# Kernel tuning notes

Measured on AMD Instinct MI355X. Metric: run time of the kernel, lower is better.

## Reference

```python
import jax, jax.numpy as jnp
import numpy as np

MAX_WAVELENGTH = 1000.0

def _sine_pos(n, d):
    # keras_nlp SinePositionEncoding with max_wavelength=1000
    pos = jnp.arange(n, dtype=jnp.float32)
    i = jnp.arange(d)
    timescales = (1.0 / MAX_WAVELENGTH) ** ((2 * (i // 2)).astype(jnp.float32) / d)
    ang = pos[:, None] * timescales[None, :]  # (n, d)
    return jnp.where(i % 2 == 0, jnp.sin(ang), jnp.cos(ang))


def setup_inputs() -> dict:
    key = jax.random.key(0)
    ks = jax.random.split(key, 6)
    B, N, D, H, O = 4, 2048, 512, 8, 64
    inputs = jax.random.normal(ks[0], (B, N, D), jnp.float32)
    mem = jax.random.normal(ks[1], (B, H, O, O), jnp.float32) * 0.02
    # z accumulates sums of (elu(k)+1) > 0, so keep it positive
    z = jax.random.uniform(ks[2], (B, H, O), jnp.float32) + 1.0
    attn_kernel = jax.random.normal(ks[3], (D, H, O, 3), jnp.float32) * (1.0 / np.sqrt(D))
    out_kernel = jax.random.normal(ks[4], (O, H, O), jnp.float32) * (1.0 / np.sqrt(O * H))
    beta = jnp.zeros((1,), jnp.float32)
    return dict(inputs=inputs, mem=mem, z=z, attn_kernel=attn_kernel,
                out_kernel=out_kernel, beta=beta)


def reference(inputs, mem, z, attn_kernel, out_kernel, beta):
    B, N, D = inputs.shape
    x = inputs + _sine_pos(N, D)[None].astype(inputs.dtype)
    # fused QKV projection: (B,N,H,dims,3)
    kvq = jnp.einsum('bni,ihok->bnhok', x, attn_kernel)
    k, v, q = kvq[..., 0], kvq[..., 1], kvq[..., 2]
    # linear-attention memory readout
    q_elu = jax.nn.elu(q) + 1.0
    num = jnp.einsum('bhdo,bnhd->bnho', mem, q_elu)
    den = jnp.einsum('bhd,bnhd->bnh', z, q_elu)[..., None] + 1e-8
    A_mem = num / den
    # delta-rule state update
    k_elu = jax.nn.elu(k) + 1.0
    next_mem = mem + jnp.einsum('bnhz,bnho->bhzo', k_elu, v - A_mem)
    next_z = z + k_elu.sum(axis=1)
    # causal softmax attention over the chunk
    scale = jnp.sqrt(jnp.asarray(D, inputs.dtype))
    qk = jnp.einsum('bnho,bkho->bhnk', q, k) / scale
    mask = -(1.0 - jnp.tril(jnp.ones((N, N), inputs.dtype))) * 1e10
    A_soft = jax.nn.softmax(qk + mask, axis=-1)
    A_dot = jnp.einsum('bhnk,bkho->bnho', A_soft, v)
    # sigmoid-gated mix + output projection
    g = jax.nn.sigmoid(beta)  # (1,) broadcasts
    A = g * A_mem + (1.0 - g) * A_dot
    out = jnp.einsum('bnhi,iho->bno', A, out_kernel)
    return out, next_mem, next_z
```

## Files before the change

### kernel.cpp

```cpp
#include <hip/hip_runtime.h>
#include <hip/hip_bf16.h>
#include <math.h>

#define BB 4
#define SEQ 2048
#define DIM 512
#define NH 8
#define HD 64

typedef __attribute__((ext_vector_type(8))) short short8;
typedef __attribute__((ext_vector_type(4))) float f32x4;
typedef __attribute__((ext_vector_type(2))) unsigned int u32x2;
typedef __attribute__((address_space(3))) const ushort lds_cushort;

static __device__ inline ushort f2bf(float f) {
    __hip_bfloat16 h = __float2bfloat16(f);
    union { __hip_bfloat16 h; ushort u; } cv;
    cv.h = h;
    return cv.u;
}
static __device__ inline float bf2f(ushort u) {
    return __uint_as_float((uint)u << 16);
}

#define GLOAD16(g, l)                                                          \
    __builtin_amdgcn_global_load_lds(                                          \
        (const __attribute__((address_space(1))) uint32_t*)(g),                \
        (__attribute__((address_space(3))) uint32_t*)(l), 16, 0, 0)

static __device__ __forceinline__ u32x2 tr16_b64(lds_cushort* p) {
    u32x2 r;
    asm volatile("ds_read_b64_tr_b16 %0, %1" : "=v"(r) : "v"(p) : "memory");
    return r;
}

__global__ __launch_bounds__(256) void pos_add_bf16_kernel(const float* __restrict__ in,
                                                           ushort* __restrict__ xbf) {
    int idx = blockIdx.x * 256 + threadIdx.x;
    int p = idx & 255;
    int n = (idx >> 8) & 2047;
    float e = (float)(2 * p) * (1.0f / 512.0f);
    float ts = __expf(-6.907755278982137f * e);
    float arev = (float)n * (ts * 0.15915494309189535f);
    float f = arev - floorf(arev);
    float s = __builtin_amdgcn_sinf(f);
    float c = __builtin_amdgcn_cosf(f);
    float2 v = *(const float2*)(in + (size_t)idx * 2);
    uint pack = (uint)f2bf(v.x + s) | ((uint)f2bf(v.y + c) << 16);
    ((uint*)xbf)[idx] = pack;
}

__global__ __launch_bounds__(256) void wprep_kernel(const float* __restrict__ w,
                                                    ushort* __restrict__ wt,
                                                    const float* __restrict__ wo,
                                                    ushort* __restrict__ wobf) {
    int bid = blockIdx.x;
    int t = threadIdx.x;
    if (bid < 96) {
        __shared__ float tile[64][129];
        int ib = bid & 7;
        int jb = bid >> 3;
        #pragma unroll
        for (int u = 0; u < 8; ++u) {
            int idx = u * 1024 + t * 4;
            int r = idx >> 7, j = idx & 127;
            float4 v = *(const float4*)(w + (size_t)(ib * 64 + r) * 1536 + jb * 128 + j);
            tile[r][j] = v.x; tile[r][j + 1] = v.y; tile[r][j + 2] = v.z; tile[r][j + 3] = v.w;
        }
        __syncthreads();
        int j = t >> 1;
        int rh = (t & 1) * 32;
        int jg = jb * 128 + j;
        int h = jg / 192;
        int rem = jg - h * 192;
        int o = rem / 3;
        int c = rem - o * 3;
        int nrow = c * 512 + h * 64 + o;
        #pragma unroll
        for (int s8 = 0; s8 < 4; ++s8) {
            short8 pk;
            #pragma unroll
            for (int q = 0; q < 8; ++q) pk[q] = (short)f2bf(tile[rh + s8 * 8 + q][j]);
            *(short8*)(wt + (size_t)nrow * 512 + ib * 64 + rh + s8 * 8) = pk;
        }
    } else {
        int g = (bid - 96) * 256 + t;
        int o2 = g >> 9, k = g & 511;
        int h = k >> 6, i = k & 63;
        wobf[g] = f2bf(wo[(size_t)i * 512 + h * 64 + o2]);
    }
}

__global__ __launch_bounds__(256) void qkv_mfma_kernel(const ushort* __restrict__ xbf,
                                                       const ushort* __restrict__ wt,
                                                       ushort* __restrict__ kbf,
                                                       ushort* __restrict__ vbf,
                                                       ushort* __restrict__ qbf) {
    __shared__ __align__(16) ushort As[128 * 64];
    __shared__ __align__(16) ushort Bs[128 * 64];
    int t = threadIdx.x;
    int w = t >> 6, lane = t & 63, l15 = lane & 15, lg = lane >> 4;
    int wr = w >> 1, wc = w & 1;
    int m0 = blockIdx.x * 128;
    int by = blockIdx.y;
    int n0 = by * 128;
    int sw = l15 & 7;
    f32x4 acc[4][4] = {};

    int rowp[4], colp[4];
    #pragma unroll
    for (int p = 0; p < 4; ++p) {
        int ch = t + 256 * p;
        rowp[p] = ch >> 3;
        colp[p] = (((ch & 7) ^ (rowp[p] & 7))) * 8;
    }

    for (int k0 = 0; k0 < 512; k0 += 64) {
        __syncthreads();
        #pragma unroll
        for (int p = 0; p < 4; ++p)
            GLOAD16(xbf + (size_t)(m0 + rowp[p]) * 512 + k0 + colp[p], As + (t + 256 * p) * 8);
        #pragma unroll
        for (int p = 0; p < 4; ++p)
            GLOAD16(wt + (size_t)(n0 + rowp[p]) * 512 + k0 + colp[p], Bs + (t + 256 * p) * 8);
        __syncthreads();
        #pragma unroll
        for (int ks = 0; ks < 2; ++ks) {
            short8 af[4], bf[4];
            #pragma unroll
            for (int mi = 0; mi < 4; ++mi)
                af[mi] = *(const short8*)&As[(wr * 64 + mi * 16 + l15) * 64 + ((ks * 4 + lg) ^ sw) * 8];
            #pragma unroll
            for (int ni = 0; ni < 4; ++ni)
                bf[ni] = *(const short8*)&Bs[(wc * 64 + ni * 16 + l15) * 64 + ((ks * 4 + lg) ^ sw) * 8];
            #pragma unroll
            for (int mi = 0; mi < 4; ++mi)
                #pragma unroll
                for (int ni = 0; ni < 4; ++ni)
                    acc[mi][ni] = __builtin_amdgcn_mfma_f32_16x16x32_bf16(af[mi], bf[ni], acc[mi][ni], 0, 0, 0);
        }
    }

    ushort* dst = (by < 4) ? kbf : (by < 8) ? vbf : qbf;
    int ho0 = (by & 3) * 128 + wc * 64;
    int mb = m0 + wr * 64;
    #pragma unroll
    for (int mi = 0; mi < 4; ++mi)
        #pragma unroll
        for (int ni = 0; ni < 4; ++ni)
            #pragma unroll
            for (int r = 0; r < 4; ++r)
                dst[(size_t)(mb + mi * 16 + lg * 4 + r) * 512 + ho0 + ni * 16 + l15] =
                    f2bf(acc[mi][ni][r]);
}

__global__ __launch_bounds__(256) void amem_mfma_kernel(const ushort* __restrict__ qbf,
                                                        const float* __restrict__ mem,
                                                        const float* __restrict__ zin,
                                                        ushort* __restrict__ ambf) {
    int bid = blockIdx.x;
    int nt = bid & 7;
    int h = (bid >> 3) & 7;
    int b = bid >> 6;
    __shared__ __align__(16) ushort bt_s[80 * 64];
    int t = threadIdx.x;
    int w = t >> 6, lane = t & 63, l15 = lane & 15, lg = lane >> 4;

    {
        int d = t >> 2;
        int o0 = (t & 3) * 16;
        const float* msrc = mem + (size_t)(b * 8 + h) * 4096 + (size_t)d * 64 + o0;
        #pragma unroll
        for (int j = 0; j < 16; ++j) {
            int o = o0 + j;
            int c = (d >> 3) ^ (o & 7);
            bt_s[(o * 8 + c) * 8 + (d & 7)] = f2bf(msrc[j]);
        }
        if (t < 64) {
            bt_s[(64 * 8 + (t >> 3)) * 8 + (t & 7)] = f2bf(zin[(b * 8 + h) * 64 + t]);
        }
    }
    __syncthreads();

    int sw = l15 & 7;
    short8 bfr[5][2];
    #pragma unroll
    for (int n = 0; n < 5; ++n) {
        const ushort* br = &bt_s[(n * 16 + l15) * 64];
        bfr[n][0] = *(const short8*)&br[(lg ^ sw) * 8];
        bfr[n][1] = *(const short8*)&br[((4 + lg) ^ sw) * 8];
    }

    int rowbase = b * 2048 + nt * 256 + w * 64;
    f32x4 acc[4][5] = {};
    #pragma unroll
    for (int m = 0; m < 4; ++m) {
        const ushort* qrow = qbf + (size_t)(rowbase + m * 16 + l15) * 512 + h * 64;
        short8 q0 = *(const short8*)(qrow + lg * 8);
        short8 q1 = *(const short8*)(qrow + 32 + lg * 8);
        short8 a0, a1;
        #pragma unroll
        for (int j = 0; j < 8; ++j) {
            float f0 = bf2f((ushort)q0[j]);
            float f1 = bf2f((ushort)q1[j]);
            a0[j] = (short)f2bf(f0 > 0.f ? f0 + 1.f : __expf(f0));
            a1[j] = (short)f2bf(f1 > 0.f ? f1 + 1.f : __expf(f1));
        }
        #pragma unroll
        for (int n = 0; n < 5; ++n) {
            acc[m][n] = __builtin_amdgcn_mfma_f32_16x16x32_bf16(a0, bfr[n][0], acc[m][n], 0, 0, 0);
            acc[m][n] = __builtin_amdgcn_mfma_f32_16x16x32_bf16(a1, bfr[n][1], acc[m][n], 0, 0, 0);
        }
    }

    #pragma unroll
    for (int m = 0; m < 4; ++m) {
        float inv[4];
        #pragma unroll
        for (int r = 0; r < 4; ++r) {
            float d = __shfl(acc[m][4][r], (lane & 48));
            inv[r] = 1.f / (d + 1e-8f);
        }
        #pragma unroll
        for (int r = 0; r < 4; ++r) {
            ushort* dst = ambf + (size_t)(rowbase + m * 16 + lg * 4 + r) * 512 + h * 64;
            #pragma unroll
            for (int n = 0; n < 4; ++n)
                dst[n * 16 + l15] = f2bf(acc[m][n][r] * inv[r]);
        }
    }
}

__global__ __launch_bounds__(256) void delta_part_kernel(const ushort* __restrict__ kbf,
                                                         const ushort* __restrict__ vbf,
                                                         const ushort* __restrict__ ambf,
                                                         float* __restrict__ part,
                                                         float* __restrict__ zpart) {
    int bid = blockIdx.x;
    int bh = bid & 31;
    int chunk = bid >> 5;
    int h = bh & 7, b = bh >> 3;
    __shared__ __align__(16) float ke_s[2048];
    __shared__ __align__(16) float vm_s[2048];
    int t = threadIdx.x;
    int tx = t & 15, ty = t >> 4;
    float acc[4][4] = {};
    float nz = 0.f;
    int nbase = chunk * 256;
    for (int n0 = 0; n0 < 256; n0 += 32) {
        {
            int nn = t >> 3, cc = (t & 7) * 8;
            size_t g = (size_t)(b * 2048 + nbase + n0 + nn) * 512 + h * 64 + cc;
            short8 k8 = *(const short8*)(kbf + g);
            short8 v8 = *(const short8*)(vbf + g);
            short8 a8 = *(const short8*)(ambf + g);
            #pragma unroll
            for (int j = 0; j < 8; ++j) {
                float kv = bf2f((ushort)k8[j]);
                ke_s[t * 8 + j] = kv > 0.f ? kv + 1.f : __expf(kv);
                vm_s[t * 8 + j] = bf2f((ushort)v8[j]) - bf2f((ushort)a8[j]);
            }
        }
        __syncthreads();
        #pragma unroll
        for (int nn = 0; nn < 32; ++nn) {
            float4 ka4 = *(const float4*)&ke_s[nn * 64 + ty * 4];
            float4 vv4 = *(const float4*)&vm_s[nn * 64 + tx * 4];
            float ka[4] = {ka4.x, ka4.y, ka4.z, ka4.w};
            float vv[4] = {vv4.x, vv4.y, vv4.z, vv4.w};
            #pragma unroll
            for (int i = 0; i < 4; ++i)
                #pragma unroll
                for (int j = 0; j < 4; ++j) acc[i][j] += ka[i] * vv[j];
        }
        if (t < 64) {
            #pragma unroll
            for (int nn = 0; nn < 32; ++nn) nz += ke_s[nn * 64 + t];
        }
        __syncthreads();
    }
    float* pdst = part + (size_t)bid * 4096;
    #pragma unroll
    for (int i = 0; i < 4; ++i)
        #pragma unroll
        for (int j = 0; j < 4; ++j)
            pdst[(ty * 4 + i) * 64 + tx * 4 + j] = acc[i][j];
    if (t < 64) zpart[bid * 64 + t] = nz;
}

__global__ __launch_bounds__(256) void delta_reduce_kernel(const float* __restrict__ part,
                                                           const float* __restrict__ zpart,
                                                           const float* __restrict__ mem,
                                                           const float* __restrict__ zin,
                                                           float* __restrict__ out_mem,
                                                           float* __restrict__ out_z) {
    int bh = blockIdx.x;
    int t = threadIdx.x;
    #pragma unroll
    for (int q = 0; q < 4; ++q) {
        int e = t * 16 + q * 4;
        float4 acc = *(const float4*)(mem + (size_t)bh * 4096 + e);
        #pragma unroll
        for (int c = 0; c < 8; ++c) {
            float4 pv = *(const float4*)(part + (size_t)(c * 32 + bh) * 4096 + e);
            acc.x += pv.x; acc.y += pv.y; acc.z += pv.z; acc.w += pv.w;
        }
        *(float4*)(out_mem + (size_t)bh * 4096 + e) = acc;
    }
    if (t < 64) {
        float z = zin[bh * 64 + t];
        #pragma unroll
        for (int c = 0; c < 8; ++c) z += zpart[(c * 32 + bh) * 64 + t];
        out_z[bh * 64 + t] = z;
    }
}

__global__ __launch_bounds__(256, 2) void flash5_kernel(const ushort* __restrict__ qbf,
                                                        const ushort* __restrict__ kbf,
                                                        const ushort* __restrict__ vbf,
                                                        ushort* __restrict__ adbf) {
    int bid0 = blockIdx.x;
    int bid = (bid0 & 7) * 64 + (bid0 >> 3);
    int i = bid & 15;
    int h = (bid >> 4) & 7;
    int b = bid >> 7;
    __shared__ __align__(16) ushort k_s[2][4096];
    __shared__ __align__(16) ushort v_s[2][4096];
    __shared__ __align__(16) ushort p_s[4][1024];
    int t = threadIdx.x;
    int w = t >> 6, lane = t & 63, l15 = lane & 15, lg = lane >> 4;
    const int rA = i, rB = 31 - i;
    const int sw = l15 & 7;
    const float C = 0.06375875f;

    const ushort* qbase = qbf + (size_t)(b * 2048) * 512 + h * 64 + lg * 8;
    short8 qfA[2], qfB[2];
    #pragma unroll
    for (int c = 0; c < 2; ++c) {
        short8 ra = *(const short8*)(qbase + (size_t)(rA * 64 + w * 16 + l15) * 512 + c * 32);
        short8 rb = *(const short8*)(qbase + (size_t)(rB * 64 + w * 16 + l15) * 512 + c * 32);
        #pragma unroll
        for (int j = 0; j < 8; ++j) {
            qfA[c][j] = (short)f2bf(bf2f((ushort)ra[j]) * C);
            qfB[c][j] = (short)f2bf(bf2f((ushort)rb[j]) * C);
        }
    }
    f32x4 oA[4] = {}, oB[4] = {};
    f32x4 lA = {0.f, 0.f, 0.f, 0.f}, lB = {0.f, 0.f, 0.f, 0.f};

    int ch0 = t, ch1 = t + 256;
    int krow0 = ch0 >> 3, ksc0 = (ch0 & 7) ^ (krow0 & 7);
    int krow1 = ch1 >> 3, ksc1 = (ch1 & 7) ^ (krow1 & 7);
    int vd0 = ch0 >> 7, vn0 = (ch0 >> 1) & 63, vh0 = ch0 & 1;
    int vd1 = ch1 >> 7, vn1 = (ch1 >> 1) & 63, vh1 = ch1 & 1;
    const ushort* kbase = kbf + (size_t)(b * 2048) * 512 + h * 64;
    const ushort* vbase = vbf + (size_t)(b * 2048) * 512 + h * 64;
    ushort* pw = &p_s[w][0];

    short8 ones;
    #pragma unroll
    for (int j = 0; j < 8; ++j) ones[j] = (short)0x3F80;

    short8 kf[4][2], vf[4][2];

    auto STAGE = [&](int buf, int kt) {
        GLOAD16(kbase + (size_t)(kt * 64 + krow0) * 512 + ksc0 * 8, &k_s[buf][ch0 * 8]);
        GLOAD16(kbase + (size_t)(kt * 64 + krow1) * 512 + ksc1 * 8, &k_s[buf][ch1 * 8]);
        GLOAD16(vbase + (size_t)(kt * 64 + vn0) * 512 + vd0 * 16 + vh0 * 8, &v_s[buf][ch0 * 8]);
        GLOAD16(vbase + (size_t)(kt * 64 + vn1) * 512 + vd1 * 16 + vh1 * 8, &v_s[buf][ch1 * 8]);
    };

    auto proc = [&](const short8* qf, f32x4* oo, f32x4& ll, int rt, int kt) {
        f32x4 s[4];
        #pragma unroll
        for (int t4 = 0; t4 < 4; ++t4) {
            f32x4 z = {0.f, 0.f, 0.f, 0.f};
            z = __builtin_amdgcn_mfma_f32_16x16x32_bf16(qf[0], kf[t4][0], z, 0, 0, 0);
            z = __builtin_amdgcn_mfma_f32_16x16x32_bf16(qf[1], kf[t4][1], z, 0, 0, 0);
            s[t4] = z;
        }
        if (kt == rt) {
            #pragma unroll
            for (int t4 = 0; t4 < 4; ++t4) {
                int colb = t4 * 16 + l15;
                int rowb = w * 16 + lg * 4;
                #pragma unroll
                for (int r = 0; r < 4; ++r)
                    if (colb > rowb + r) s[t4][r] = -1e30f;
            }
        }
        #pragma unroll
        for (int t4 = 0; t4 < 4; ++t4) {
            union { ushort u[4]; u32x2 d; } pk;
            #pragma unroll
            for (int r = 0; r < 4; ++r)
                pk.u[r] = f2bf(__builtin_amdgcn_exp2f(s[t4][r]));
            *(u32x2*)&pw[(t4 * 16 + l15) * 16 + lg * 4] = pk.d;
        }
        u32x2 praw0, praw1, praw2, praw3;
        {
            lds_cushort* pb = (lds_cushort*)&pw[l15];
            praw0 = tr16_b64(pb + (lg * 8 + 0) * 16);
            praw1 = tr16_b64(pb + (lg * 8 + 4) * 16);
            praw2 = tr16_b64(pb + (32 + lg * 8 + 0) * 16);
            praw3 = tr16_b64(pb + (32 + lg * 8 + 4) * 16);
        }
        asm volatile("s_waitcnt lgkmcnt(0)" ::: "memory");
        __builtin_amdgcn_sched_barrier(0);
        union { u32x2 d[2]; short8 s8; } up0, up1;
        up0.d[0] = praw0; up0.d[1] = praw1;
        up1.d[0] = praw2; up1.d[1] = praw3;
        short8 pf0 = up0.s8, pf1 = up1.s8;
        ll = __builtin_amdgcn_mfma_f32_16x16x32_bf16(pf0, ones, ll, 0, 0, 0);
        ll = __builtin_amdgcn_mfma_f32_16x16x32_bf16(pf1, ones, ll, 0, 0, 0);
        #pragma unroll
        for (int dt = 0; dt < 4; ++dt) {
            oo[dt] = __builtin_amdgcn_mfma_f32_16x16x32_bf16(pf0, vf[dt][0], oo[dt], 0, 0, 0);
            oo[dt] = __builtin_amdgcn_mfma_f32_16x16x32_bf16(pf1, vf[dt][1], oo[dt], 0, 0, 0);
        }
    };

    STAGE(0, 0);
    for (int kt = 0; kt <= rB; ++kt) {
        int cur = kt & 1;
        __builtin_amdgcn_s_barrier();
        if (kt < rB) {
            STAGE(cur ^ 1, kt + 1);
            asm volatile("s_waitcnt vmcnt(4)" ::: "memory");
        } else {
            asm volatile("s_waitcnt vmcnt(0)" ::: "memory");
        }
        __builtin_amdgcn_s_barrier();
        #pragma unroll
        for (int t4 = 0; t4 < 4; ++t4) {
            const ushort* kr = &k_s[cur][(t4 * 16 + l15) * 64];
            kf[t4][0] = *(const short8*)&kr[(lg ^ sw) * 8];
            kf[t4][1] = *(const short8*)&kr[((4 + lg) ^ sw) * 8];
        }
        u32x2 vraw[4][4];
        #pragma unroll
        for (int dt = 0; dt < 4; ++dt) {
            lds_cushort* vb = (lds_cushort*)&v_s[cur][dt * 1024 + l15];
            vraw[dt][0] = tr16_b64(vb + (lg * 8 + 0) * 16);
            vraw[dt][1] = tr16_b64(vb + (lg * 8 + 4) * 16);
            vraw[dt][2] = tr16_b64(vb + (32 + lg * 8 + 0) * 16);
            vraw[dt][3] = tr16_b64(vb + (32 + lg * 8 + 4) * 16);
        }
        asm volatile("s_waitcnt lgkmcnt(0)" ::: "memory");
        __builtin_amdgcn_sched_barrier(0);
        #pragma unroll
        for (int dt = 0; dt < 4; ++dt) {
            union { u32x2 d[2]; short8 s8; } u0, u1;
            u0.d[0] = vraw[dt][0]; u0.d[1] = vraw[dt][1];
            u1.d[0] = vraw[dt][2]; u1.d[1] = vraw[dt][3];
            vf[dt][0] = u0.s8;
            vf[dt][1] = u1.s8;
        }
        proc(qfB, oB, lB, rB, kt);
        if (kt <= rA) proc(qfA, oA, lA, rA, kt);
    }

    auto fin = [&](f32x4* oo, f32x4& ll, int rt) {
        #pragma unroll
        for (int r = 0; r < 4; ++r) {
            float inv = 1.f / ll[r];
            ushort* dst = adbf + (size_t)(b * 2048 + rt * 64 + w * 16 + lg * 4 + r) * 512 + h * 64;
            #pragma unroll
            for (int dt = 0; dt < 4; ++dt)
                dst[dt * 16 + l15] = f2bf(oo[dt][r] * inv);
        }
    };
    fin(oA, lA, rA);
    fin(oB, lB, rB);
}

__global__ __launch_bounds__(256) void outproj_mfma_kernel(const ushort* __restrict__ ambf,
                                                           const ushort* __restrict__ adbf,
                                                           const ushort* __restrict__ wobf,
                                                           const float* __restrict__ beta,
                                                           float* __restrict__ out) {
    __shared__ __align__(16) ushort W_s[64 * 512];
    __shared__ __align__(16) ushort A_s[32 * 64];
    int t = threadIdx.x;
    int w = t >> 6, lane = t & 63, l15 = lane & 15, lg = lane >> 4;
    int msub = w & 1, nh = w >> 1;
    int m0 = blockIdx.x * 32;
    float g = 1.f / (1.f + __expf(-beta[0]));
    float gi = 1.f - g;

    #pragma unroll
    for (int p = 0; p < 16; ++p) {
        int ch = p * 256 + t;
        int row = ch >> 6, c = ch & 63;
        int cs = c ^ (row & 7);
        GLOAD16(wobf + (size_t)row * 512 + cs * 8, W_s + ch * 8);
    }

    int ar = t >> 3, ac = t & 7;
    int sw = l15 & 7;
    f32x4 acc[2] = {};

    for (int ks = 0; ks < 8; ++ks) {
        size_t gofs = (size_t)(m0 + ar) * 512 + ks * 64 + ac * 8;
        short8 a8 = *(const short8*)(ambf + gofs);
        short8 d8 = *(const short8*)(adbf + gofs);
        short8 x0;
        #pragma unroll
        for (int j = 0; j < 8; ++j)
            x0[j] = (short)f2bf(g * bf2f((ushort)a8[j]) + gi * bf2f((ushort)d8[j]));
        if (ks) __syncthreads();
        *(short8*)&A_s[(ar * 8 + (ac ^ (ar & 7))) * 8] = x0;
        __syncthreads();

        const ushort* arow = &A_s[(msub * 16 + l15) * 64];
        short8 af0 = *(const short8*)&arow[(lg ^ sw) * 8];
        short8 af1 = *(const short8*)&arow[((4 + lg) ^ sw) * 8];
        #pragma unroll
        for (int ni = 0; ni < 2; ++ni) {
            const ushort* wrow = &W_s[(nh * 32 + ni * 16 + l15) * 512];
            short8 bf0 = *(const short8*)&wrow[(ks * 8 + (lg ^ sw)) * 8];
            short8 bf1 = *(const short8*)&wrow[(ks * 8 + ((4 + lg) ^ sw)) * 8];
            acc[ni] = __builtin_amdgcn_mfma_f32_16x16x32_bf16(af0, bf0, acc[ni], 0, 0, 0);
            acc[ni] = __builtin_amdgcn_mfma_f32_16x16x32_bf16(af1, bf1, acc[ni], 0, 0, 0);
        }
    }

    #pragma unroll
    for (int ni = 0; ni < 2; ++ni)
        #pragma unroll
        for (int r = 0; r < 4; ++r)
            out[(size_t)(m0 + msub * 16 + lg * 4 + r) * 64 + nh * 32 + ni * 16 + l15] = acc[ni][r];
}

extern "C" void kernel_launch(void* const* d_in, const int* in_sizes, int n_in,
                              void* d_out, int out_size, void* d_ws, size_t ws_size,
                              hipStream_t stream) {
    const float* inputs = (const float*)d_in[0];
    const float* mem    = (const float*)d_in[1];
    const float* zin    = (const float*)d_in[2];
    const float* attnk  = (const float*)d_in[3];
    const float* outk   = (const float*)d_in[4];
    const float* beta   = (const float*)d_in[5];
    float* out = (float*)d_out;
    float* ws  = (float*)d_ws;

    ushort* am_bf = (ushort*)ws;
    ushort* ad_bf = (ushort*)(ws + 2097152);
    ushort* kbf   = (ushort*)(ws + 4194304);
    ushort* vbf   = (ushort*)(ws + 6291456);
    ushort* qbf   = (ushort*)(ws + 8388608);
    ushort* xbf   = (ushort*)(ws + 12582912);
    ushort* wtbf  = (ushort*)(ws + 14680064);
    ushort* wobf  = (ushort*)(ws + 15073280);
    float*  part  = ws + 15089664;
    float*  zpart = ws + 16138240;

    float* out_main = out;
    float* out_mem  = out + 524288;
    float* out_z    = out + 655360;

    pos_add_bf16_kernel<<<8192, 256, 0, stream>>>(inputs, xbf);
    wprep_kernel<<<224, 256, 0, stream>>>(attnk, wtbf, outk, wobf);
    qkv_mfma_kernel<<<dim3(64, 12), 256, 0, stream>>>(xbf, wtbf, kbf, vbf, qbf);
    amem_mfma_kernel<<<256, 256, 0, stream>>>(qbf, mem, zin, am_bf);
    delta_part_kernel<<<256, 256, 0, stream>>>(kbf, vbf, am_bf, part, zpart);
    delta_reduce_kernel<<<32, 256, 0, stream>>>(part, zpart, mem, zin, out_mem, out_z);
    flash5_kernel<<<512, 256, 0, stream>>>(qbf, kbf, vbf, ad_bf);
    outproj_mfma_kernel<<<256, 256, 0, stream>>>(am_bf, ad_bf, wobf, beta, out_main);
}
```

Measured before the change: 180.3 us.

## Split flash attention KV range across two blocks with combine kernel

```diff
diff --git a/kernel.cpp b/kernel.cpp
--- a/kernel.cpp
+++ b/kernel.cpp
@@ -315,15 +315,19 @@
     }
 }
 
-__global__ __launch_bounds__(256, 2) void flash5_kernel(const ushort* __restrict__ qbf,
+__global__ __launch_bounds__(256, 2) void flash6_kernel(const ushort* __restrict__ qbf,
                                                         const ushort* __restrict__ kbf,
                                                         const ushort* __restrict__ vbf,
-                                                        ushort* __restrict__ adbf) {
+                                                        ushort* __restrict__ adbf,
+                                                        float* __restrict__ pO,
+                                                        float* __restrict__ pl) {
     int bid0 = blockIdx.x;
-    int bid = (bid0 & 7) * 64 + (bid0 >> 3);
-    int i = bid & 15;
-    int h = (bid >> 4) & 7;
-    int b = bid >> 7;
+    int bid = (bid0 & 7) * 128 + (bid0 >> 3);
+    int half = bid >> 9;
+    int rem = bid & 511;
+    int i = rem & 15;
+    int h = (rem >> 4) & 7;
+    int b = rem >> 7;
     __shared__ __align__(16) ushort k_s[2][4096];
     __shared__ __align__(16) ushort v_s[2][4096];
     __shared__ __align__(16) ushort p_s[4][1024];
@@ -332,17 +336,23 @@
     const int rA = i, rB = 31 - i;
     const int sw = l15 & 7;
     const float C = 0.06375875f;
+    int kt0 = half ? 16 : 0;
+    int kt1 = half ? rB : 15;
 
     const ushort* qbase = qbf + (size_t)(b * 2048) * 512 + h * 64 + lg * 8;
     short8 qfA[2], qfB[2];
     #pragma unroll
     for (int c = 0; c < 2; ++c) {
-        short8 ra = *(const short8*)(qbase + (size_t)(rA * 64 + w * 16 + l15) * 512 + c * 32);
         short8 rb = *(const short8*)(qbase + (size_t)(rB * 64 + w * 16 + l15) * 512 + c * 32);
         #pragma unroll
-        for (int j = 0; j < 8; ++j) {
-            qfA[c][j] = (short)f2bf(bf2f((ushort)ra[j]) * C);
-            qfB[c][j] = (short)f2bf(bf2f((ushort)rb[j]) * C);
+        for (int j = 0; j < 8; ++j) qfB[c][j] = (short)f2bf(bf2f((ushort)rb[j]) * C);
+    }
+    if (!half) {
+        #pragma unroll
+        for (int c = 0; c < 2; ++c) {
+            short8 ra = *(const short8*)(qbase + (size_t)(rA * 64 + w * 16 + l15) * 512 + c * 32);
+            #pragma unroll
+            for (int j = 0; j < 8; ++j) qfA[c][j] = (short)f2bf(bf2f((ushort)ra[j]) * C);
         }
     }
     f32x4 oA[4] = {}, oB[4] = {};
@@ -420,11 +430,11 @@
         }
     };
 
-    STAGE(0, 0);
-    for (int kt = 0; kt <= rB; ++kt) {
-        int cur = kt & 1;
+    STAGE(0, kt0);
+    for (int kt = kt0; kt <= kt1; ++kt) {
+        int cur = (kt - kt0) & 1;
         __builtin_amdgcn_s_barrier();
-        if (kt < rB) {
+        if (kt < kt1) {
             STAGE(cur ^ 1, kt + 1);
             asm volatile("s_waitcnt vmcnt(4)" ::: "memory");
         } else {
@@ -457,21 +467,70 @@
             vf[dt][1] = u1.s8;
         }
         proc(qfB, oB, lB, rB, kt);
-        if (kt <= rA) proc(qfA, oA, lA, rA, kt);
-    }
-
-    auto fin = [&](f32x4* oo, f32x4& ll, int rt) {
+        if (!half && kt <= rA) proc(qfA, oA, lA, rA, kt);
+    }
+
+    if (!half) {
         #pragma unroll
         for (int r = 0; r < 4; ++r) {
-            float inv = 1.f / ll[r];
-            ushort* dst = adbf + (size_t)(b * 2048 + rt * 64 + w * 16 + lg * 4 + r) * 512 + h * 64;
+            float inv = 1.f / lA[r];
+            ushort* dst = adbf + (size_t)(b * 2048 + rA * 64 + w * 16 + lg * 4 + r) * 512 + h * 64;
             #pragma unroll
             for (int dt = 0; dt < 4; ++dt)
-                dst[dt * 16 + l15] = f2bf(oo[dt][r] * inv);
-        }
-    };
-    fin(oA, lA, rA);
-    fin(oB, lB, rB);
+                dst[dt * 16 + l15] = f2bf(oA[dt][r] * inv);
+        }
+    }
+    {
+        int slot = rem * 2 + half;
+        float* od = pO + (size_t)slot * 4096;
+        #pragma unroll
+        for (int dt = 0; dt < 4; ++dt)
+            #pragma unroll
+            for (int r = 0; r < 4; ++r)
+                od[(w * 16 + lg * 4 + r) * 64 + dt * 16 + l15] = oB[dt][r];
+        if (l15 == 0) {
+            #pragma unroll
+            for (int r = 0; r < 4; ++r)
+                pl[slot * 64 + w * 16 + lg * 4 + r] = lB[r];
+        }
+    }
+}
+
+__global__ __launch_bounds__(256) void flash_combine_kernel(const float* __restrict__ pO,
+                                                            const float* __restrict__ pl,
+                                                            ushort* __restrict__ adbf) {
+    int rem = blockIdx.x;
+    int i = rem & 15;
+    int h = (rem >> 4) & 7;
+    int b = rem >> 7;
+    int rB = 31 - i;
+    int t = threadIdx.x;
+    int r = t >> 2, c0 = (t & 3) * 16;
+    size_t s0 = (size_t)(rem * 2) * 4096, s1 = s0 + 4096;
+    float l = pl[(rem * 2) * 64 + r] + pl[(rem * 2 + 1) * 64 + r];
+    float inv = 1.f / l;
+    ushort* dst = adbf + (size_t)(b * 2048 + rB * 64 + r) * 512 + h * 64 + c0;
+    short8 pk0, pk1;
+    #pragma unroll
+    for (int j = 0; j < 2; ++j) {
+        float4 a = *(const float4*)(pO + s0 + r * 64 + c0 + j * 4);
+        float4 bq = *(const float4*)(pO + s1 + r * 64 + c0 + j * 4);
+        pk0[j * 4 + 0] = (short)f2bf((a.x + bq.x) * inv);
+        pk0[j * 4 + 1] = (short)f2bf((a.y + bq.y) * inv);
+        pk0[j * 4 + 2] = (short)f2bf((a.z + bq.z) * inv);
+        pk0[j * 4 + 3] = (short)f2bf((a.w + bq.w) * inv);
+    }
+    #pragma unroll
+    for (int j = 0; j < 2; ++j) {
+        float4 a = *(const float4*)(pO + s0 + r * 64 + c0 + 8 + j * 4);
+        float4 bq = *(const float4*)(pO + s1 + r * 64 + c0 + 8 + j * 4);
+        pk1[j * 4 + 0] = (short)f2bf((a.x + bq.x) * inv);
+        pk1[j * 4 + 1] = (short)f2bf((a.y + bq.y) * inv);
+        pk1[j * 4 + 2] = (short)f2bf((a.z + bq.z) * inv);
+        pk1[j * 4 + 3] = (short)f2bf((a.w + bq.w) * inv);
+    }
+    *(short8*)dst = pk0;
+    *(short8*)(dst + 8) = pk1;
 }
 
 __global__ __launch_bounds__(256) void outproj_mfma_kernel(const ushort* __restrict__ ambf,
@@ -554,6 +613,8 @@
     ushort* wobf  = (ushort*)(ws + 15073280);
     float*  part  = ws + 15089664;
     float*  zpart = ws + 16138240;
+    float*  pO    = ws + 16154624;
+    float*  pl    = ws + 20348928;
 
     float* out_main = out;
     float* out_mem  = out + 524288;
@@ -565,6 +626,7 @@
     amem_mfma_kernel<<<256, 256, 0, stream>>>(qbf, mem, zin, am_bf);
     delta_part_kernel<<<256, 256, 0, stream>>>(kbf, vbf, am_bf, part, zpart);
     delta_reduce_kernel<<<32, 256, 0, stream>>>(part, zpart, mem, zin, out_mem, out_z);
-    flash5_kernel<<<512, 256, 0, stream>>>(qbf, kbf, vbf, ad_bf);
+    flash6_kernel<<<1024, 256, 0, stream>>>(qbf, kbf, vbf, ad_bf, pO, pl);
+    flash_combine_kernel<<<512, 256, 0, stream>>>(pO, pl, ad_bf);
     outproj_mfma_kernel<<<256, 256, 0, stream>>>(am_bf, ad_bf, wobf, beta, out_main);
 }
```

Measured after the change: 198.5 us. 1.1x slower.
